# Performance work log

Measured on AMD Instinct MI355X. Metric: run time of the kernel, lower is better.

## Reference

```python
import jax, jax.numpy as jnp
import numpy as np
from math import sqrt

N = 8192      # points
I = 16        # in_channels
H = 64        # hidden_units
O = 64        # out_channels
CUTS = 8      # conv MLP intermediate width
RADIUS = 9.0
GROUPS = 4    # GroupNorm groups
BLK = 128     # i-block size for tiled pairwise reduction (KeOps-style)


def _leaky(x):
    return jnp.where(x >= 0, x, 0.2 * x)


def _group_norm(f, w, b, eps=1e-5):
    # torch GroupNorm applied to (1, C, N): stats per group over (C//G channels x N points)
    n, c = f.shape
    g = f.reshape(n, GROUPS, c // GROUPS)
    m = g.mean(axis=(0, 2), keepdims=True)
    v = ((g - m) ** 2).mean(axis=(0, 2), keepdims=True)
    g = (g - m) * jax.lax.rsqrt(v + eps)
    return g.reshape(n, c) * w + b


def setup_inputs() -> dict:
    key = jax.random.key(0)
    ks = jax.random.split(key, 20)
    U = lambda k, s, lim: jax.random.uniform(k, s, minval=-lim, maxval=lim)
    points = jax.random.normal(ks[0], (N, 3), dtype=jnp.float32)
    nuv = jax.random.normal(ks[1], (N, 3, 3), dtype=jnp.float32)
    features = jax.random.normal(ks[2], (N, I), dtype=jnp.float32)
    # net_in (torch Linear default init)
    W_in1 = U(ks[3], (H, I), 1 / np.sqrt(I)); b_in1 = U(ks[4], (H,), 1 / np.sqrt(I))
    W_in2 = U(ks[5], (H, H), 1 / np.sqrt(H)); b_in2 = U(ks[6], (H,), 1 / np.sqrt(H))
    # conv MLP with custom init from the module
    A1 = jax.random.normal(ks[7], (CUTS, 3), dtype=jnp.float32)
    B1 = jax.random.uniform(ks[8], (CUTS,)) * 0.8 * jnp.sqrt((A1 ** 2).sum(-1))
    A2 = U(ks[9], (H, CUTS), 1 / np.sqrt(CUTS))
    B2 = jax.random.normal(ks[10], (H,)) * 0.5 * jnp.sqrt((A2 ** 2).sum(-1))
    # net_out
    W_out1 = U(ks[11], (O, H), 1 / np.sqrt(H)); b_out1 = U(ks[12], (O,), 1 / np.sqrt(H))
    W_out2 = U(ks[13], (O, O), 1 / np.sqrt(O)); b_out2 = U(ks[14], (O,), 1 / np.sqrt(O))
    return {
        "points": points, "nuv": nuv, "features": features,
        "W_in1": W_in1, "b_in1": b_in1, "W_in2": W_in2, "b_in2": b_in2,
        "gn_in_w": jnp.ones((H,), jnp.float32), "gn_in_b": jnp.zeros((H,), jnp.float32),
        "A1": A1, "B1": B1, "A2": A2, "B2": B2,
        "W_out1": W_out1, "b_out1": b_out1, "W_out2": W_out2, "b_out2": b_out2,
        "gn_out_w": jnp.ones((O,), jnp.float32), "gn_out_b": jnp.zeros((O,), jnp.float32),
    }


def _forward(points, nuv, features, W_in1, b_in1, W_in2, b_in2, gn_in_w, gn_in_b,
             A1, B1, A2, B2, W_out1, b_out1, W_out2, b_out2, gn_out_w, gn_out_b):
    # 1. net_in + GroupNorm
    f = _leaky(features @ W_in1.T + b_in1)
    f = _leaky(f @ W_in2.T + b_in2)
    f = _group_norm(f, gn_in_w, gn_in_b)          # (N, H)
    # 2. quasi-geodesic interaction, tiled over i-blocks (KeOps-style)
    pts = points / (sqrt(2.0) * RADIUS)
    normals = jax.lax.stop_gradient(nuv[:, 0, :])  # n_j is detached in the original
    nblk = N // BLK

    def body(carry, blk):
        xi, nuvi = blk                              # (B,3), (B,3,3)
        ni = nuvi[:, 0, :]                          # (B,3) n_i (not detached)
        diff = pts[None, :, :] - xi[:, None, :]     # (B,N,3) x_j - x_i
        dn = ni @ normals.T                         # (B,N) <n_i, n_j>
        d2 = (diff ** 2).sum(-1) * (2.0 - dn) ** 2  # pseudo-geodesic squared dist
        w = jnp.exp(-d2)                            # Gaussian window
        X = jnp.einsum('bij,bnj->bni', nuvi, diff)  # coords in local basis (B,N,3)
        h = jax.nn.relu(jnp.einsum('bnj,cj->bnc', X, A1) + B1)   # (B,N,CUTS)
        g = jax.nn.relu(jnp.einsum('bnc,hc->bnh', h, A2) + B2)   # (B,N,H)
        out = jnp.einsum('bn,bnh,nh->bh', w, g, f)  # sum_j w_ij * conv(P_ij) * f_j
        return carry, out

    _, outs = jax.lax.scan(
        body, None, (pts.reshape(nblk, BLK, 3), nuv.reshape(nblk, BLK, 3, 3)))
    f2 = outs.reshape(N, H)
    # 3. net_out + GroupNorm
    f2 = _leaky(f2 @ W_out1.T + b_out1)
    f2 = _leaky(f2 @ W_out2.T + b_out2)
    f2 = _group_norm(f2, gn_out_w, gn_out_b)       # (N, O)
    return f2


def reference(points, nuv, features, W_in1, b_in1, W_in2, b_in2, gn_in_w, gn_in_b,
              A1, B1, A2, B2, W_out1, b_out1, W_out2, b_out2, gn_out_w, gn_out_b):
    return _forward(points, nuv, features, W_in1, b_in1, W_in2, b_in2, gn_in_w, gn_in_b,
                    A1, B1, A2, B2, W_out1, b_out1, W_out2, b_out2, gn_out_w, gn_out_b)
```

## Files before the change

kernel.cpp:

```cpp
#include <hip/hip_runtime.h>
#include <hip/hip_bf16.h>
#include <stdint.h>


#define N_PTS   8192
#define CHUNK   64
#define NCHUNK  (N_PTS / CHUNK)
#define WPB     8
#define PSCALE  0.07856742013183861f
#define GN_CNT  (N_PTS * 16)

#define OFF_POINTS 0
#define OFF_NUV    24576
#define OFF_FEAT   98304
#define OFF_WIN1   229376
#define OFF_BIN1   230400
#define OFF_WIN2   230464
#define OFF_BIN2   234560
#define OFF_GNIW   234624
#define OFF_GNIB   234688
#define OFF_A1     234752
#define OFF_B1     234776
#define OFF_A2     234784
#define OFF_B2     235296
#define OFF_WOUT1  235360
#define OFF_BOUT1  239456
#define OFF_WOUT2  239520
#define OFF_BOUT2  243616
#define OFF_GNOW   243680
#define OFF_GNOB   243744
#define CVT_TOTAL  243808
#define NSEG 19

typedef _Float16 half2_t __attribute__((ext_vector_type(2)));
typedef _Float16 f16x8   __attribute__((ext_vector_type(8)));
typedef float    f32x16  __attribute__((ext_vector_type(16)));

struct InPtrs { const void* p[NSEG]; };

__device__ __forceinline__ float rfl(float x) {
  return __int_as_float(__builtin_amdgcn_readfirstlane(__float_as_int(x)));
}
__device__ __forceinline__ float leaky(float x) { return x > 0.f ? x : 0.2f * x; }

#if __has_builtin(__builtin_amdgcn_cvt_pkrtz)
__device__ __forceinline__ half2_t pk16(float a, float b) {
  return __builtin_bit_cast(half2_t, __builtin_amdgcn_cvt_pkrtz(a, b));
}
#else
__device__ __forceinline__ half2_t pk16(float a, float b) {
  half2_t r; r.x = (_Float16)a; r.y = (_Float16)b; return r;
}
#endif

__global__ __launch_bounds__(256) void prep_kernel(InPtrs ptrs, float* dst,
                                                   float* gstats) {
  if (blockIdx.x == 0 && threadIdx.x < 16) gstats[threadIdx.x] = 0.f;
  const uint32_t w0 = ((const uint32_t*)ptrs.p[7])[0];
  const bool bf = (w0 != 0x3F800000u);
  const int CUM[NSEG + 1] = {0, 24576, 98304, 229376, 230400, 230464, 234560,
                             234624, 234688, 234752, 234776, 234784, 235296,
                             235360, 239456, 239520, 243616, 243680, 243744,
                             243808};
  for (int e = blockIdx.x * 256 + threadIdx.x; e < CVT_TOTAL;
       e += gridDim.x * 256) {
    int s = 0;
#pragma unroll
    for (int i = 1; i < NSEG; ++i) s += (e >= CUM[i]) ? 1 : 0;
    const int rem = e - CUM[s];
    float v = bf ? __bfloat162float(((const __hip_bfloat16*)ptrs.p[s])[rem])
                 : ((const float*)ptrs.p[s])[rem];
    if (s == 0) v *= PSCALE;
    dst[e] = v;
  }
}

__global__ __launch_bounds__(256) void mlp_in_kernel(
    const float* __restrict__ pool, float* __restrict__ fbuf) {
  __shared__ float ls[4][64];
  const int t = threadIdx.x, nl = t >> 6, h = t & 63;
  const int n = blockIdx.x * 4 + nl;
  const float4* fr = (const float4*)(pool + OFF_FEAT + n * 16);
  const float4* w1 = (const float4*)(pool + OFF_WIN1 + h * 16);
  float a = pool[OFF_BIN1 + h];
#pragma unroll
  for (int k = 0; k < 4; ++k) {
    const float4 x = fr[k], w = w1[k];
    a = fmaf(x.x, w.x, a); a = fmaf(x.y, w.y, a);
    a = fmaf(x.z, w.z, a); a = fmaf(x.w, w.w, a);
  }
  ls[nl][h] = leaky(a);
  __syncthreads();
  const float4* w2 = (const float4*)(pool + OFF_WIN2 + h * 64);
  const float4* lr = (const float4*)&ls[nl][0];
  float c = pool[OFF_BIN2 + h];
#pragma unroll
  for (int k = 0; k < 16; ++k) {
    const float4 x = lr[k], w = w2[k];
    c = fmaf(x.x, w.x, c); c = fmaf(x.y, w.y, c);
    c = fmaf(x.z, w.z, c); c = fmaf(x.w, w.w, c);
  }
  fbuf[n * 64 + h] = leaky(c);
}

__global__ __launch_bounds__(256) void mlp_out_kernel(
    const float* __restrict__ cbuf, const float* __restrict__ pool,
    float* __restrict__ obuf) {
  __shared__ float ls[4][64];
  const int t = threadIdx.x, nl = t >> 6, h = t & 63;
  const int n = blockIdx.x * 4 + nl;
  const float4* cr = (const float4*)(cbuf + n * 64);
  const float4* w1 = (const float4*)(pool + OFF_WOUT1 + h * 64);
  float a = pool[OFF_BOUT1 + h];
#pragma unroll
  for (int k = 0; k < 16; ++k) {
    const float4 x = cr[k], w = w1[k];
    a = fmaf(x.x, w.x, a); a = fmaf(x.y, w.y, a);
    a = fmaf(x.z, w.z, a); a = fmaf(x.w, w.w, a);
  }
  ls[nl][h] = leaky(a);
  __syncthreads();
  const float4* w2 = (const float4*)(pool + OFF_WOUT2 + h * 64);
  const float4* lr = (const float4*)&ls[nl][0];
  float c = pool[OFF_BOUT2 + h];
#pragma unroll
  for (int k = 0; k < 16; ++k) {
    const float4 x = lr[k], w = w2[k];
    c = fmaf(x.x, w.x, c); c = fmaf(x.y, w.y, c);
    c = fmaf(x.z, w.z, c); c = fmaf(x.w, w.w, c);
  }
  obuf[n * 64 + h] = leaky(c);
}

__global__ __launch_bounds__(256) void gn_stats_kernel(
    const float* __restrict__ buf, float* __restrict__ gstats) {
  __shared__ float red[8];
  const int t = threadIdx.x;
  const int g = (t & 63) >> 4;
  if (t < 8) red[t] = 0.f;
  float s = 0.f, q = 0.f;
  for (int idx = blockIdx.x * 256 + t; idx < N_PTS * 64; idx += 64 * 256) {
    const float v = buf[idx];
    s += v; q = fmaf(v, v, q);
  }
  __syncthreads();
  atomicAdd(&red[g], s);
  atomicAdd(&red[4 + g], q);
  __syncthreads();
  if (t < 8) atomicAdd(&gstats[t], red[t]);
}

__global__ __launch_bounds__(256) void gn_apply_kernel(
    float* __restrict__ buf, const float* __restrict__ gstats,
    const float* __restrict__ pool) {
  const int idx = blockIdx.x * 256 + threadIdx.x;
  const int h = idx & 63, g = h >> 4;
  const float m = gstats[g] * (1.f / GN_CNT);
  const float v = gstats[4 + g] * (1.f / GN_CNT) - m * m;
  const float rs = rsqrtf(fmaxf(v, 0.f) + 1e-5f);
  buf[idx] = fmaf((buf[idx] - m) * rs, pool[OFF_GNIW + h], pool[OFF_GNIB + h]);
}

__global__ __launch_bounds__(256) void gn_apply_out_kernel(
    const float* __restrict__ buf, const float* __restrict__ gstats,
    const float* __restrict__ pool, void* __restrict__ out,
    const uint32_t* __restrict__ dref) {
  const bool bf = (dref[0] != 0x3F800000u);
  const int idx = blockIdx.x * 256 + threadIdx.x;
  const int h = idx & 63, g = h >> 4;
  const float m = gstats[g] * (1.f / GN_CNT);
  const float v = gstats[4 + g] * (1.f / GN_CNT) - m * m;
  const float rs = rsqrtf(fmaxf(v, 0.f) + 1e-5f);
  const float r = fmaf((buf[idx] - m) * rs, pool[OFF_GNOW + h], pool[OFF_GNOB + h]);
  if (bf) ((__hip_bfloat16*)out)[idx] = __float2bfloat16(r);
  else    ((float*)out)[idx] = r;
}

__global__ __launch_bounds__(512) void conv_kernel(
    const float* __restrict__ pool, const float* __restrict__ fbuf,
    float* __restrict__ cbuf) {
  __shared__ float  f_s[CHUNK * 64];
  __shared__ float4 hcA[WPB][2][64];

  const int t = threadIdx.x;
  const int wv = t >> 6, lane = t & 63;
  const int b = blockIdx.x * WPB + wv;
  const int half = lane >> 5;
  const int l31 = lane & 31;

  const float pbx = rfl(pool[OFF_POINTS + b * 3 + 0]);
  const float pby = rfl(pool[OFF_POINTS + b * 3 + 1]);
  const float pbz = rfl(pool[OFF_POINTS + b * 3 + 2]);
  float nb[9];
#pragma unroll
  for (int i = 0; i < 9; ++i) nb[i] = rfl(pool[OFF_NUV + b * 9 + i]);
  float a1v[24], b1v[8];
#pragma unroll
  for (int i = 0; i < 24; ++i) a1v[i] = rfl(pool[OFF_A1 + i]);
#pragma unroll
  for (int i = 0; i < 8; ++i)  b1v[i] = rfl(pool[OFF_B1 + i]);

  f16x8 bfrag[2];
#pragma unroll
  for (int ht = 0; ht < 2; ++ht) {
    const int h = l31 + 32 * ht;
#pragma unroll
    for (int i = 0; i < 8; ++i) {
      const float v = (half == 0) ? pool[OFF_A2 + h * 8 + i]
                                  : ((i == 0) ? pool[OFF_B2 + h] : 0.f);
      bfrag[ht][i] = (_Float16)v;
    }
  }

  {
    float4 z4; z4.x = 0.f; z4.y = 0.f; z4.z = 0.f; z4.w = 0.f;
    hcA[wv][half][l31 + 32] = z4;
  }

  const f32x16 kzero = {0.f, 0.f, 0.f, 0.f, 0.f, 0.f, 0.f, 0.f,
                        0.f, 0.f, 0.f, 0.f, 0.f, 0.f, 0.f, 0.f};

  float acc0 = 0.f, acc1 = 0.f;
  const float4* fg4 = (const float4*)fbuf;

  for (int c = 0; c < NCHUNK; ++c) {
    const float4 fv0 = fg4[c * 1024 + t];
    const float4 fv1 = fg4[c * 1024 + t + 512];
    const int n = c * CHUNK + lane;
    const float px = pool[OFF_POINTS + n * 3 + 0];
    const float py = pool[OFF_POINTS + n * 3 + 1];
    const float pz = pool[OFF_POINTS + n * 3 + 2];
    const float nx = pool[OFF_NUV + n * 9 + 0];
    const float ny = pool[OFF_NUV + n * 9 + 1];
    const float nz = pool[OFF_NUV + n * 9 + 2];

    __syncthreads();
    ((float4*)f_s)[t]       = fv0;
    ((float4*)f_s)[t + 512] = fv1;

    const float dx = px - pbx, dy = py - pby, dz = pz - pbz;
    const float X0 = fmaf(nb[0], dx, fmaf(nb[1], dy, nb[2] * dz));
    const float X1 = fmaf(nb[3], dx, fmaf(nb[4], dy, nb[5] * dz));
    const float X2 = fmaf(nb[6], dx, fmaf(nb[7], dy, nb[8] * dz));
    const float dn = fmaf(nb[0], nx, fmaf(nb[1], ny, nb[2] * nz));
    const float dd = fmaf(dx, dx, fmaf(dy, dy, dz * dz));
    const float tt = 2.f - dn;
    const float w = __expf(-dd * tt * tt);

    float hc[8];
#pragma unroll
    for (int cc = 0; cc < 8; ++cc)
      hc[cc] = w * fmaxf(fmaf(X0, a1v[cc * 3 + 0],
                         fmaf(X1, a1v[cc * 3 + 1],
                         fmaf(X2, a1v[cc * 3 + 2], b1v[cc]))), 0.f);
    float4 lo;
    lo.x = __builtin_bit_cast(float, pk16(hc[0], hc[1]));
    lo.y = __builtin_bit_cast(float, pk16(hc[2], hc[3]));
    lo.z = __builtin_bit_cast(float, pk16(hc[4], hc[5]));
    lo.w = __builtin_bit_cast(float, pk16(hc[6], hc[7]));
    hcA[wv][lane >> 5][l31] = lo;
    ((float*)&hcA[wv][lane >> 5][l31 + 32])[0] =
        __builtin_bit_cast(float, pk16(w, 0.f));

    __syncthreads();

#pragma unroll
    for (int jt = 0; jt < 2; ++jt) {
      const float4 av = hcA[wv][jt][lane];
      const f16x8 af = __builtin_bit_cast(f16x8, av);
      const int fbase = (32 * jt + 4 * half) * 64 + l31;
#pragma unroll
      for (int ht = 0; ht < 2; ++ht) {
        const f32x16 D = __builtin_amdgcn_mfma_f32_32x32x16_f16(
            af, bfrag[ht], kzero, 0, 0, 0);
        const float* fb = &f_s[fbase + 32 * ht];
        float a = (ht == 0) ? acc0 : acc1;
#pragma unroll
        for (int r = 0; r < 16; ++r) {
          const float fj = fb[((r & 3) + 8 * (r >> 2)) * 64];
          a = fmaf(fj, fmaxf(D[r], 0.f), a);
        }
        if (ht == 0) acc0 = a; else acc1 = a;
      }
    }
  }

  acc0 += __shfl_xor(acc0, 32, 64);
  acc1 += __shfl_xor(acc1, 32, 64);
  if (lane < 32) {
    cbuf[b * 64 + l31]      = acc0;
    cbuf[b * 64 + l31 + 32] = acc1;
  }
}

extern "C" void kernel_launch(void* const* d_in, const int* in_sizes, int n_in,
                              void* d_out, int out_size, void* d_ws, size_t ws_size,
                              hipStream_t stream) {
  (void)in_sizes; (void)n_in; (void)out_size; (void)ws_size;
  const uint32_t* dref = (const uint32_t*)d_in[7];

  float* pool   = (float*)d_ws;
  float* fbuf   = pool + CVT_TOTAL;
  float* cbuf   = fbuf + N_PTS * 64;
  float* gstats = cbuf + N_PTS * 64;

  InPtrs ptrs;
  for (int i = 0; i < NSEG; ++i) ptrs.p[i] = d_in[i];

  prep_kernel<<<256, 256, 0, stream>>>(ptrs, pool, gstats);
  mlp_in_kernel<<<N_PTS / 4, 256, 0, stream>>>(pool, fbuf);
  gn_stats_kernel<<<64, 256, 0, stream>>>(fbuf, gstats);
  gn_apply_kernel<<<N_PTS * 64 / 256, 256, 0, stream>>>(fbuf, gstats, pool);
  conv_kernel<<<N_PTS / WPB, 512, 0, stream>>>(pool, fbuf, cbuf);
  mlp_out_kernel<<<N_PTS / 4, 256, 0, stream>>>(cbuf, pool, fbuf);
  gn_stats_kernel<<<64, 256, 0, stream>>>(fbuf, gstats + 8);
  gn_apply_out_kernel<<<N_PTS * 64 / 256, 256, 0, stream>>>(
      fbuf, gstats + 8, pool, d_out, dref);
}
```

Measured before the change: 804.3 us.

## Switch conv MFMA from 32x32x16 to 16x16x32 tiles with padded feature LDS

Restructures the pairwise conv inner loop to use 16x16x32 f16 MFMA over four j-tiles and four h-tiles instead of 32x32x16 over two each. The hidden-activation staging buffer is re-laid out to match, and the K dimension is padded through a shared zero vector for the upper lane groups. The feature tile in LDS gets a padded row stride of 68 to avoid bank conflicts. The intent is cheaper MFMA issue and fewer conflicting LDS reads, at the cost of more MFMA calls, half of whose K lanes are zeros, plus an extra shuffle-reduction step.

```diff
diff --git a/kernel.cpp b/kernel.cpp
--- a/kernel.cpp
+++ b/kernel.cpp
@@ -9,6 +9,7 @@
 #define WPB     8
 #define PSCALE  0.07856742013183861f
 #define GN_CNT  (N_PTS * 16)
+#define FS_STRIDE 68
 
 #define OFF_POINTS 0
 #define OFF_NUV    24576
@@ -34,7 +35,7 @@
 
 typedef _Float16 half2_t __attribute__((ext_vector_type(2)));
 typedef _Float16 f16x8   __attribute__((ext_vector_type(8)));
-typedef float    f32x16  __attribute__((ext_vector_type(16)));
+typedef float    f32x4   __attribute__((ext_vector_type(4)));
 
 struct InPtrs { const void* p[NSEG]; };
 
@@ -179,14 +180,15 @@
 __global__ __launch_bounds__(512) void conv_kernel(
     const float* __restrict__ pool, const float* __restrict__ fbuf,
     float* __restrict__ cbuf) {
-  __shared__ float  f_s[CHUNK * 64];
-  __shared__ float4 hcA[WPB][2][64];
+  __shared__ float  f_s[CHUNK * FS_STRIDE];
+  __shared__ float4 hcA[WPB][4][32];
+  __shared__ float4 zero4_s;
 
   const int t = threadIdx.x;
   const int wv = t >> 6, lane = t & 63;
   const int b = blockIdx.x * WPB + wv;
-  const int half = lane >> 5;
-  const int l31 = lane & 31;
+  const int kg  = lane >> 4;
+  const int l15 = lane & 15;
 
   const float pbx = rfl(pool[OFF_POINTS + b * 3 + 0]);
   const float pby = rfl(pool[OFF_POINTS + b * 3 + 1]);
@@ -200,27 +202,30 @@
 #pragma unroll
   for (int i = 0; i < 8; ++i)  b1v[i] = rfl(pool[OFF_B1 + i]);
 
-  f16x8 bfrag[2];
-#pragma unroll
-  for (int ht = 0; ht < 2; ++ht) {
-    const int h = l31 + 32 * ht;
+  f16x8 bfrag[4];
+#pragma unroll
+  for (int ht = 0; ht < 4; ++ht) {
+    const int h = 16 * ht + l15;
 #pragma unroll
     for (int i = 0; i < 8; ++i) {
-      const float v = (half == 0) ? pool[OFF_A2 + h * 8 + i]
-                                  : ((i == 0) ? pool[OFF_B2 + h] : 0.f);
+      float v = 0.f;
+      if (kg == 0) v = pool[OFF_A2 + h * 8 + i];
+      else if (kg == 1 && i == 0) v = pool[OFF_B2 + h];
       bfrag[ht][i] = (_Float16)v;
     }
   }
 
   {
     float4 z4; z4.x = 0.f; z4.y = 0.f; z4.z = 0.f; z4.w = 0.f;
-    hcA[wv][half][l31 + 32] = z4;
-  }
-
-  const f32x16 kzero = {0.f, 0.f, 0.f, 0.f, 0.f, 0.f, 0.f, 0.f,
-                        0.f, 0.f, 0.f, 0.f, 0.f, 0.f, 0.f, 0.f};
-
-  float acc0 = 0.f, acc1 = 0.f;
+    if (lane < 32) {
+#pragma unroll
+      for (int jt = 0; jt < 4; ++jt) hcA[wv][jt][lane] = z4;
+    }
+    if (t == 0) zero4_s = z4;
+  }
+
+  const f32x4 kzero = {0.f, 0.f, 0.f, 0.f};
+  float acc[4] = {0.f, 0.f, 0.f, 0.f};
   const float4* fg4 = (const float4*)fbuf;
 
   for (int c = 0; c < NCHUNK; ++c) {
@@ -235,8 +240,8 @@
     const float nz = pool[OFF_NUV + n * 9 + 2];
 
     __syncthreads();
-    ((float4*)f_s)[t]       = fv0;
-    ((float4*)f_s)[t + 512] = fv1;
+    ((float4*)f_s)[(t >> 4) * 17 + (t & 15)]        = fv0;
+    ((float4*)f_s)[((t >> 4) + 32) * 17 + (t & 15)] = fv1;
 
     const float dx = px - pbx, dy = py - pby, dz = pz - pbz;
     const float X0 = fmaf(nb[0], dx, fmaf(nb[1], dy, nb[2] * dz));
@@ -258,38 +263,38 @@
     lo.y = __builtin_bit_cast(float, pk16(hc[2], hc[3]));
     lo.z = __builtin_bit_cast(float, pk16(hc[4], hc[5]));
     lo.w = __builtin_bit_cast(float, pk16(hc[6], hc[7]));
-    hcA[wv][lane >> 5][l31] = lo;
-    ((float*)&hcA[wv][lane >> 5][l31 + 32])[0] =
+    hcA[wv][lane >> 4][l15] = lo;
+    ((float*)&hcA[wv][lane >> 4][16 + l15])[0] =
         __builtin_bit_cast(float, pk16(w, 0.f));
 
     __syncthreads();
 
 #pragma unroll
-    for (int jt = 0; jt < 2; ++jt) {
-      const float4 av = hcA[wv][jt][lane];
-      const f16x8 af = __builtin_bit_cast(f16x8, av);
-      const int fbase = (32 * jt + 4 * half) * 64 + l31;
-#pragma unroll
-      for (int ht = 0; ht < 2; ++ht) {
-        const f32x16 D = __builtin_amdgcn_mfma_f32_32x32x16_f16(
+    for (int jt = 0; jt < 4; ++jt) {
+      const float4* ap = (kg < 2) ? &hcA[wv][jt][kg * 16 + l15] : &zero4_s;
+      const f16x8 af = __builtin_bit_cast(f16x8, *ap);
+      const int fbase = (16 * jt + kg * 4) * FS_STRIDE + l15;
+#pragma unroll
+      for (int ht = 0; ht < 4; ++ht) {
+        const f32x4 D = __builtin_amdgcn_mfma_f32_16x16x32_f16(
             af, bfrag[ht], kzero, 0, 0, 0);
-        const float* fb = &f_s[fbase + 32 * ht];
-        float a = (ht == 0) ? acc0 : acc1;
-#pragma unroll
-        for (int r = 0; r < 16; ++r) {
-          const float fj = fb[((r & 3) + 8 * (r >> 2)) * 64];
-          a = fmaf(fj, fmaxf(D[r], 0.f), a);
-        }
-        if (ht == 0) acc0 = a; else acc1 = a;
+        const float* fb = &f_s[fbase + 16 * ht];
+#pragma unroll
+        for (int r = 0; r < 4; ++r)
+          acc[ht] = fmaf(fb[r * FS_STRIDE], fmaxf(D[r], 0.f), acc[ht]);
       }
     }
   }
 
-  acc0 += __shfl_xor(acc0, 32, 64);
-  acc1 += __shfl_xor(acc1, 32, 64);
-  if (lane < 32) {
-    cbuf[b * 64 + l31]      = acc0;
-    cbuf[b * 64 + l31 + 32] = acc1;
+#pragma unroll
+  for (int ht = 0; ht < 4; ++ht) {
+    acc[ht] += __shfl_xor(acc[ht], 16, 64);
+    acc[ht] += __shfl_xor(acc[ht], 32, 64);
+  }
+  if (lane < 16) {
+#pragma unroll
+    for (int ht = 0; ht < 4; ++ht)
+      cbuf[b * 64 + 16 * ht + lane] = acc[ht];
   }
 }
 
```

Result: faster. 699.2 us (-13.1%).
